# Kernel tuning notes

Hardware: AMD Instinct MI355X
Metric: run time of the kernel (lower is better)

The kernel has to match this reference:

```python
import jax, jax.numpy as jnp
import numpy as np

B, S = 1024, 512
V, E, H, T = 50000, 300, 800, 50


def setup_inputs() -> dict:
    key = jax.random.key(0)
    ks = jax.random.split(key, 8)
    ids = jax.random.randint(ks[0], (B, S), 0, V, dtype=jnp.int64 if jax.config.jax_enable_x64 else jnp.int32)
    return {
        "ids": ids,
        "rho": jax.random.normal(ks[1], (V, E), jnp.float32) * 0.02,
        "alpha": jax.random.normal(ks[2], (T, E), jnp.float32) * 0.02,
        "W1": jax.random.normal(ks[3], (E, H), jnp.float32) * 0.05,
        "b1": jnp.zeros((H,), jnp.float32),
        "Wmu": jax.random.normal(ks[4], (H, T), jnp.float32) * 0.05,
        "bmu": jnp.zeros((T,), jnp.float32),
        "Wlv": jax.random.normal(ks[5], (H, T), jnp.float32) * 0.05,
        "blv": jnp.zeros((T,), jnp.float32),
    }


def reference(ids, rho, alpha, W1, b1, Wmu, bmu, Wlv, blv):
    b, s = ids.shape
    v = rho.shape[0]
    # bag-of-words histogram: scatter-add instead of dense one_hot+reduce_sum
    bows = jnp.zeros((b, v), rho.dtype).at[jnp.arange(b)[:, None], ids].add(1.0)
    # zero out special tokens 1 and 2 (original: x * (1 - sum(one_hot([1,2]))))
    bows = bows.at[:, jnp.array([1, 2])].set(0.0)
    normal_bows = bows / jnp.sum(bows, axis=-1, keepdims=True)
    # encoder (eval mode: dropout is identity)
    x = jnp.einsum('bv,ve->be', normal_bows, rho)
    h = jax.nn.relu(x @ W1 + b1)
    mu_theta = h @ Wmu + bmu
    logsigma_theta = h @ Wlv + blv
    kl_theta = -0.5 * jnp.sum(1.0 + logsigma_theta - mu_theta**2 - jnp.exp(logsigma_theta), axis=-1)
    # reparameterize (eval/inference mode): z = mu
    theta = jax.nn.softmax(mu_theta, axis=-1)  # [B, T]
    beta = jax.nn.softmax(jnp.einsum('te,ve->tv', alpha, rho), axis=-1)  # [T, V]
    lookup = jnp.log(theta @ beta + 1e-5)  # [B, V]
    recon_loss = -jnp.sum(lookup * bows, axis=-1)
    loss = jnp.mean(recon_loss) + jnp.mean(kl_theta)
    return theta, loss
```

## Files before the change

kernel.cpp:

```cpp
#include <hip/hip_runtime.h>
#include <math.h>


#define Bn 1024
#define Sn 512
#define Vn 50000
#define En 300
#define Hn 800
#define Tn 50
#define KP 320
#define BSTR 64
#define W1FRAG_N (50 * 10 * 64 * 8)
#define WFRAG_N  (8 * 25 * 64 * 8)
#define NRANGE 8
#define K4B 3128

typedef __bf16 bf16x8 __attribute__((ext_vector_type(8)));
typedef float  f32x4  __attribute__((ext_vector_type(4)));
typedef float  f32x2  __attribute__((ext_vector_type(2)));

__device__ __forceinline__ float waveReduceSum(float v) {
    #pragma unroll
    for (int off = 32; off > 0; off >>= 1) v += __shfl_xor(v, off, 64);
    return v;
}
__device__ __forceinline__ float waveReduceMax(float v) {
    #pragma unroll
    for (int off = 32; off > 0; off >>= 1) v = fmaxf(v, __shfl_xor(v, off, 64));
    return v;
}
__device__ __forceinline__ unsigned short f2bf(float x) {
    unsigned u = __float_as_uint(x);
    return (unsigned short)((u + 0x7FFFu + ((u >> 16) & 1u)) >> 16);
}
__device__ __forceinline__ float bf_lo(unsigned u) { return __uint_as_float(u << 16); }
__device__ __forceinline__ float bf_hi(unsigned u) { return __uint_as_float(u & 0xFFFF0000u); }
__device__ __forceinline__ int lane_prefix(unsigned long long m) {
    return __builtin_amdgcn_mbcnt_hi((unsigned)(m >> 32),
           __builtin_amdgcn_mbcnt_lo((unsigned)m, 0));
}

#define PKACC(u) { \
    c0 += (f32x2){bf_lo((u).x), bf_hi((u).x)}; \
    c1 += (f32x2){bf_lo((u).y), bf_hi((u).y)}; \
    c2 += (f32x2){bf_lo((u).z), bf_hi((u).z)}; \
    c3 += (f32x2){bf_lo((u).w), bf_hi((u).w)}; }

__global__ __launch_bounds__(256) void ka2_init(
        const float* __restrict__ alpha, const float* __restrict__ W1,
        const float* __restrict__ Wmu, const float* __restrict__ Wlv,
        unsigned short* __restrict__ bfrag, unsigned short* __restrict__ w1frag,
        unsigned short* __restrict__ wfrag, float* __restrict__ topicsumR,
        float* __restrict__ loss) {
    const int gid = blockIdx.x * 256 + threadIdx.x;
    if (gid < 512) topicsumR[gid] = 0.f;
    if (gid == 520) *loss = 0.f;
    if (gid < 4 * 10 * 64 * 8) {
        int j = gid & 7;
        int lane = (gid >> 3) & 63;
        int rest = gid >> 9;
        int kt = rest % 10, w = rest / 10;
        int t = 16 * w + (lane & 15);
        int e = kt * 32 + (lane >> 4) * 8 + j;
        bfrag[gid] = (t < Tn && e < En) ? f2bf(alpha[t * En + e]) : (unsigned short)0;
    }
    if (gid < W1FRAG_N) {
        int j = gid & 7, lane = (gid >> 3) & 63, rest = gid >> 9;
        int kt = rest % 10, nt = rest / 10;
        int e = kt * 32 + (lane >> 4) * 8 + j;
        int hcol = nt * 16 + (lane & 15);
        w1frag[gid] = (e < En) ? f2bf(W1[e * Hn + hcol]) : (unsigned short)0;
    } else {
        int g2 = gid - W1FRAG_N;
        if (g2 < WFRAG_N) {
            int j = g2 & 7, lane = (g2 >> 3) & 63, rest = g2 >> 9;
            int kt = rest % 25, nt = rest / 25;
            int k = kt * 32 + (lane >> 4) * 8 + j;
            int t = (nt & 3) * 16 + (lane & 15);
            float val = 0.f;
            if (t < Tn) val = (nt < 4) ? Wmu[k * Tn + t] : Wlv[k * Tn + t];
            wfrag[g2] = f2bf(val);
        }
    }
}

__global__ __launch_bounds__(256) void kb4_beta(
        const float* __restrict__ rho, unsigned short* __restrict__ rhoh,
        const unsigned short* __restrict__ bfrag,
        unsigned int* __restrict__ betaU32, float* __restrict__ topicsumR) {
    __shared__ __align__(16) unsigned short xs[16 * 328];
    __shared__ unsigned short trans[16 * 66];
    const int x = blockIdx.x & 7;
    const int n = blockIdx.x >> 3;
    const int tile = ((x * 3125) >> 3) + n;
    if (tile >= (((x + 1) * 3125) >> 3)) return;
    const int tid = threadIdx.x;
    const int wave = tid >> 6, lane = tid & 63;
    const int quad = lane >> 4, l15 = lane & 15;
    const int v0 = tile * 16;
    for (int i = tid; i < 16 * 80; i += 256) {
        int row = i / 80, s4 = i - row * 80;
        ushort4 o = {0, 0, 0, 0};
        if (s4 < 75) {
            float4 r = *(const float4*)(rho + (size_t)(v0 + row) * En + s4 * 4);
            o.x = f2bf(r.x); o.y = f2bf(r.y); o.z = f2bf(r.z); o.w = f2bf(r.w);
        }
        *(ushort4*)&xs[row * 328 + s4 * 4] = o;
    }
    __syncthreads();
    for (int i = tid; i < 16 * 40; i += 256) {
        int row = i / 40, c8 = (i - row * 40) * 8;
        *(uint4*)(rhoh + (size_t)(v0 + row) * KP + c8) = *(const uint4*)&xs[row * 328 + c8];
    }
    const unsigned short* arow = xs + l15 * 328 + quad * 8;
    f32x4 acc = {0.f, 0.f, 0.f, 0.f};
    #pragma unroll
    for (int kt = 0; kt < 10; ++kt) {
        bf16x8 a = *(const bf16x8*)(arow + kt * 32);
        bf16x8 bv = *(const bf16x8*)(bfrag + ((wave * 10 + kt) * 64 + lane) * 8);
        acc = __builtin_amdgcn_mfma_f32_16x16x32_bf16(a, bv, acc, 0, 0, 0);
    }
    float ts = 0.f;
    #pragma unroll
    for (int r = 0; r < 4; ++r) {
        float ev = expf(acc[r]);
        ts += ev;
        trans[(quad * 4 + r) * 66 + 16 * wave + l15] = f2bf(ev);
    }
    ts += __shfl_xor(ts, 16, 64);
    ts += __shfl_xor(ts, 32, 64);
    const int t = 16 * wave + l15;
    if (lane < 16 && t < Tn)
        atomicAdd(&topicsumR[x * 64 + t], ts);
    __syncthreads();
    unsigned int* dst = betaU32 + (size_t)v0 * 32;
    const unsigned int* tr32 = (const unsigned int*)trans;
    for (int i = tid; i < 16 * 32; i += 256)
        dst[i] = tr32[(i >> 5) * 33 + (i & 31)];
}

__global__ __launch_bounds__(256) void kb1_gather(
        const unsigned short* __restrict__ rhoh, const int* __restrict__ ids,
        int* __restrict__ toks, int* __restrict__ cnt,
        float* __restrict__ xbarP) {
    __shared__ __align__(16) int sid[Sn];
    __shared__ int sfid[Sn];
    __shared__ __align__(16) float xred[4][320];
    __shared__ int scount, sfull;
    const int tid = threadIdx.x;
    const int wave = tid >> 6, lane = tid & 63;
    const int r = blockIdx.x & (NRANGE - 1), b = blockIdx.x >> 3;
    const int lo = ((r * 3125) >> 3) * 16;
    const int hi = (((r + 1) * 3125) >> 3) * 16;
    if (tid == 0) { scount = 0; sfull = 0; }
    __syncthreads();
    #pragma unroll
    for (int s0 = 0; s0 < Sn; s0 += 256) {
        int id = __builtin_nontemporal_load(&ids[b * Sn + s0 + tid]);
        bool val = (id != 1 && id != 2);
        bool inr = val && id >= lo && id < hi;
        unsigned long long mb = __ballot(inr);
        int pre = lane_prefix(mb);
        int wc = __popcll(mb);
        int base = 0;
        if (lane == 0 && wc) base = atomicAdd(&scount, wc);
        base = __shfl(base, 0, 64);
        if (inr) sid[base + pre] = id;
        if (r == 0) {
            unsigned long long fb = __ballot(val);
            int fpre = lane_prefix(fb);
            int fwc = __popcll(fb);
            int fbase = 0;
            if (lane == 0 && fwc) fbase = atomicAdd(&sfull, fwc);
            fbase = __shfl(fbase, 0, 64);
            if (val) sfid[fbase + fpre] = id;
        }
    }
    __syncthreads();
    if (r == 0) {
        const int nf = sfull;
        for (int i = tid; i < nf; i += 256) toks[b * Sn + i] = sfid[i];
        if (tid == 0) cnt[b] = nf;
    }
    const int m = scount;
    f32x2 c0 = {0.f, 0.f}, c1 = {0.f, 0.f}, c2 = {0.f, 0.f}, c3 = {0.f, 0.f};
    if (lane < 40) {
        const uint4* rb = (const uint4*)rhoh;
        int s = wave;
        for (; s + 12 < m; s += 16) {
            int i0 = sid[s], i1 = sid[s + 4], i2 = sid[s + 8], i3 = sid[s + 12];
            uint4 u0 = rb[(size_t)i0 * 40 + lane];
            uint4 u1 = rb[(size_t)i1 * 40 + lane];
            uint4 u2 = rb[(size_t)i2 * 40 + lane];
            uint4 u3 = rb[(size_t)i3 * 40 + lane];
            PKACC(u0); PKACC(u1); PKACC(u2); PKACC(u3);
        }
        for (; s < m; s += 4) {
            uint4 u = rb[(size_t)sid[s] * 40 + lane];
            PKACC(u);
        }
        float* xw = &xred[wave][lane * 8];
        *(float4*)(xw)     = (float4){c0[0], c0[1], c1[0], c1[1]};
        *(float4*)(xw + 4) = (float4){c2[0], c2[1], c3[0], c3[1]};
    }
    __syncthreads();
    float* xbp = xbarP + ((size_t)b * NRANGE + r) * KP;
    for (int c = tid; c < KP; c += 256)
        xbp[c] = xred[0][c] + xred[1][c] + xred[2][c] + xred[3][c];
}

__global__ __launch_bounds__(256) void ktail(
        const float* __restrict__ xbarP, const int* __restrict__ cnt,
        const unsigned short* __restrict__ w1frag, const float* __restrict__ b1,
        const unsigned short* __restrict__ wfrag,
        const float* __restrict__ bmu, const float* __restrict__ blv,
        float* __restrict__ theta, float* __restrict__ loss) {
    __shared__ unsigned short xs[16 * 328];
    __shared__ unsigned short hs[16 * 808];
    __shared__ float mlds[16 * 65];
    __shared__ float llds[16 * 65];
    __shared__ float invn[16];
    const int tid = threadIdx.x;
    const int wave = tid >> 6, lane = tid & 63;
    const int quad = lane >> 4, l15 = lane & 15;
    const int b0 = blockIdx.x * 16;
    if (tid < 16) invn[tid] = 1.0f / (float)cnt[b0 + tid];
    __syncthreads();
    for (int i = tid; i < 16 * (KP / 4); i += 256) {
        int row = i / (KP / 4), e4 = (i - row * (KP / 4)) * 4;
        const float* bp = xbarP + ((size_t)(b0 + row) * NRANGE) * KP + e4;
        float sx = 0.f, sy = 0.f, sz = 0.f, sw_ = 0.f;
        #pragma unroll
        for (int rr = 0; rr < NRANGE; ++rr) {
            float4 v = *(const float4*)(bp + rr * KP);
            sx += v.x; sy += v.y; sz += v.z; sw_ += v.w;
        }
        float in = invn[row];
        ushort4 o;
        o.x = f2bf(sx * in); o.y = f2bf(sy * in);
        o.z = f2bf(sz * in); o.w = f2bf(sw_ * in);
        *(ushort4*)&xs[row * 328 + e4] = o;
    }
    __syncthreads();
    {
        const unsigned short* arow = xs + l15 * 328 + quad * 8;
        for (int nt = wave; nt < 50; nt += 4) {
            f32x4 acc = {0.f, 0.f, 0.f, 0.f};
            #pragma unroll
            for (int kt = 0; kt < 10; ++kt) {
                bf16x8 a = *(const bf16x8*)(arow + kt * 32);
                bf16x8 bv = *(const bf16x8*)(w1frag + ((size_t)(nt * 10 + kt) * 64 + lane) * 8);
                acc = __builtin_amdgcn_mfma_f32_16x16x32_bf16(a, bv, acc, 0, 0, 0);
            }
            const int col = nt * 16 + l15;
            const float bias = b1[col];
            #pragma unroll
            for (int r = 0; r < 4; ++r)
                hs[(quad * 4 + r) * 808 + col] = f2bf(fmaxf(acc[r] + bias, 0.f));
        }
    }
    __syncthreads();
    {
        const unsigned short* arow = hs + l15 * 808 + quad * 8;
        f32x4 am = {0.f, 0.f, 0.f, 0.f}, al = {0.f, 0.f, 0.f, 0.f};
        #pragma unroll
        for (int kt = 0; kt < 25; ++kt) {
            bf16x8 a  = *(const bf16x8*)(arow + kt * 32);
            bf16x8 bm = *(const bf16x8*)(wfrag + ((size_t)(wave * 25 + kt) * 64 + lane) * 8);
            bf16x8 bl = *(const bf16x8*)(wfrag + ((size_t)((4 + wave) * 25 + kt) * 64 + lane) * 8);
            am = __builtin_amdgcn_mfma_f32_16x16x32_bf16(a, bm, am, 0, 0, 0);
            al = __builtin_amdgcn_mfma_f32_16x16x32_bf16(a, bl, al, 0, 0, 0);
        }
        const int t = wave * 16 + l15;
        const float bm_ = (t < Tn) ? bmu[t] : 0.f;
        const float bl_ = (t < Tn) ? blv[t] : 0.f;
        #pragma unroll
        for (int r = 0; r < 4; ++r) {
            int row = quad * 4 + r;
            mlds[row * 65 + t] = am[r] + bm_;
            llds[row * 65 + t] = al[r] + bl_;
        }
    }
    __syncthreads();
    const int tt = (lane < Tn) ? lane : (Tn - 1);
    const bool act = (lane < Tn);
    float klacc = 0.f;
    #pragma unroll
    for (int k = 0; k < 4; ++k) {
        int row = wave * 4 + k;
        float mu = mlds[row * 65 + tt];
        float lv = llds[row * 65 + tt];
        float m = waveReduceMax(act ? mu : -1e30f);
        float ex = act ? expf(mu - m) : 0.f;
        float ssum = waveReduceSum(ex);
        if (act) theta[(b0 + row) * Tn + lane] = ex / ssum;
        klacc += waveReduceSum(act ? (1.f + lv - mu * mu - expf(lv)) : 0.f);
    }
    if (lane == 0) atomicAdd(loss, -0.5f * klacc * (1.0f / (float)Bn));
}

__global__ __launch_bounds__(256) void k6_recon(
        const int* __restrict__ toks, const int* __restrict__ cnt,
        const float* __restrict__ theta, const float* __restrict__ topicsumR,
        const unsigned short* __restrict__ betaUh, float* __restrict__ loss) {
    __shared__ float sw[Tn];
    __shared__ float swred[4];
    const int b = blockIdx.x, tid = threadIdx.x;
    if (tid < Tn) {
        float z = 0.f;
        #pragma unroll
        for (int j = 0; j < 8; ++j) z += topicsumR[j * 64 + tid];
        sw[tid] = theta[b * Tn + tid] / z;
    }
    __syncthreads();
    float wr[Tn];
    #pragma unroll
    for (int t = 0; t < Tn; ++t) wr[t] = sw[t];
    float lsum = 0.f;
    const int n = cnt[b];
    for (int i = tid; i < n; i += 256) {
        int v = toks[b * Sn + i];
        const uint4* q = (const uint4*)(betaUh + (size_t)v * BSTR);
        float dot = 0.f;
        #pragma unroll
        for (int k = 0; k < 6; ++k) {
            uint4 u = q[k];
            int t = 8 * k;
            dot += wr[t]     * bf_lo(u.x) + wr[t + 1] * bf_hi(u.x);
            dot += wr[t + 2] * bf_lo(u.y) + wr[t + 3] * bf_hi(u.y);
            dot += wr[t + 4] * bf_lo(u.z) + wr[t + 5] * bf_hi(u.z);
            dot += wr[t + 6] * bf_lo(u.w) + wr[t + 7] * bf_hi(u.w);
        }
        unsigned d = ((const unsigned*)q)[24];
        dot += wr[48] * bf_lo(d) + wr[49] * bf_hi(d);
        lsum += logf(dot + 1e-5f);
    }
    float s = waveReduceSum(lsum);
    const int wave = tid >> 6, lane = tid & 63;
    if (lane == 0) swred[wave] = s;
    __syncthreads();
    if (tid == 0) {
        float tot = swred[0] + swred[1] + swred[2] + swred[3];
        atomicAdd(loss, -tot * (1.0f / (float)Bn));
    }
}

extern "C" void kernel_launch(void* const* d_in, const int* in_sizes, int n_in,
                              void* d_out, int out_size, void* d_ws, size_t ws_size,
                              hipStream_t stream) {
    const int*   ids   = (const int*)d_in[0];
    const float* rho   = (const float*)d_in[1];
    const float* alpha = (const float*)d_in[2];
    const float* W1    = (const float*)d_in[3];
    const float* b1    = (const float*)d_in[4];
    const float* Wmu   = (const float*)d_in[5];
    const float* bmu   = (const float*)d_in[6];
    const float* Wlv   = (const float*)d_in[7];
    const float* blv   = (const float*)d_in[8];

    float* theta = (float*)d_out;
    float* loss  = theta + Bn * Tn;

    char* w = (char*)d_ws;
    float* topicsumR = (float*)w;               w += 8 * 64 * 4;
    unsigned short* bfrag = (unsigned short*)w; w += 4 * 10 * 64 * 8 * 2;
    unsigned short* w1frag = (unsigned short*)w; w += (size_t)W1FRAG_N * 2;
    unsigned short* wfrag = (unsigned short*)w;  w += (size_t)WFRAG_N * 2;
    int*   cnt      = (int*)w;                  w += Bn * 4;
    int*   toks     = (int*)w;                  w += Bn * Sn * 4;
    float* xbarP    = (float*)w;                w += (size_t)Bn * NRANGE * KP * 4;
    unsigned short* rhoh = (unsigned short*)w;  w += (size_t)Vn * KP * 2;
    unsigned int* betaU32 = (unsigned int*)w;   w += (size_t)Vn * 128;

    const int k0grid = (W1FRAG_N + WFRAG_N + 255) / 256;
    ka2_init<<<k0grid, 256, 0, stream>>>(
        alpha, W1, Wmu, Wlv, bfrag, w1frag, wfrag, topicsumR, loss);
    kb4_beta<<<K4B, 256, 0, stream>>>(rho, rhoh, bfrag, betaU32, topicsumR);
    kb1_gather<<<Bn * NRANGE, 256, 0, stream>>>(rhoh, ids, toks, cnt, xbarP);
    ktail<<<64, 256, 0, stream>>>(xbarP, cnt, w1frag, b1, wfrag, bmu, blv,
                                  theta, loss);
    k6_recon<<<Bn, 256, 0, stream>>>(toks, cnt, theta, topicsumR,
                                     (const unsigned short*)betaU32, loss);
}
```

Baseline: 201.2 us.

## Fold init kernel into beta kernel and replace topic-sum atomics with per-tile partials

The separate init kernel goes away. The beta kernel now converts alpha to bf16 on the fly instead of reading precomputed fragments, and extra blocks appended to its grid build the W1 and Wmu/Wlv fragments. The per-range topic-sum atomics become plain per-tile writes, which a spare block in the tail kernel reduces. Loss zeroing moves into the gather kernel. This removes one launch and atomic contention, at the cost of redundant alpha conversion in every beta block and a serial 3125-tile reduction in one block.

Result: slower. 364.7 us (+81.3%).

```diff
diff --git a/kernel.cpp b/kernel.cpp
--- a/kernel.cpp
+++ b/kernel.cpp
@@ -14,6 +14,8 @@
 #define WFRAG_N  (8 * 25 * 64 * 8)
 #define NRANGE 8
 #define K4B 3128
+#define NTILE 3125
+#define FRAGB 1400
 
 typedef __bf16 bf16x8 __attribute__((ext_vector_type(8)));
 typedef float  f32x4  __attribute__((ext_vector_type(4)));
@@ -39,6 +41,12 @@
     return __builtin_amdgcn_mbcnt_hi((unsigned)(m >> 32),
            __builtin_amdgcn_mbcnt_lo((unsigned)m, 0));
 }
+__device__ __forceinline__ bf16x8 pack8(float4 a, float4 b) {
+    union { bf16x8 v; unsigned short s[8]; } u;
+    u.s[0] = f2bf(a.x); u.s[1] = f2bf(a.y); u.s[2] = f2bf(a.z); u.s[3] = f2bf(a.w);
+    u.s[4] = f2bf(b.x); u.s[5] = f2bf(b.y); u.s[6] = f2bf(b.z); u.s[7] = f2bf(b.w);
+    return u.v;
+}
 
 #define PKACC(u) { \
     c0 += (f32x2){bf_lo((u).x), bf_hi((u).x)}; \
@@ -46,55 +54,41 @@
     c2 += (f32x2){bf_lo((u).z), bf_hi((u).z)}; \
     c3 += (f32x2){bf_lo((u).w), bf_hi((u).w)}; }
 
-__global__ __launch_bounds__(256) void ka2_init(
-        const float* __restrict__ alpha, const float* __restrict__ W1,
-        const float* __restrict__ Wmu, const float* __restrict__ Wlv,
-        unsigned short* __restrict__ bfrag, unsigned short* __restrict__ w1frag,
-        unsigned short* __restrict__ wfrag, float* __restrict__ topicsumR,
-        float* __restrict__ loss) {
-    const int gid = blockIdx.x * 256 + threadIdx.x;
-    if (gid < 512) topicsumR[gid] = 0.f;
-    if (gid == 520) *loss = 0.f;
-    if (gid < 4 * 10 * 64 * 8) {
-        int j = gid & 7;
-        int lane = (gid >> 3) & 63;
-        int rest = gid >> 9;
-        int kt = rest % 10, w = rest / 10;
-        int t = 16 * w + (lane & 15);
-        int e = kt * 32 + (lane >> 4) * 8 + j;
-        bfrag[gid] = (t < Tn && e < En) ? f2bf(alpha[t * En + e]) : (unsigned short)0;
-    }
-    if (gid < W1FRAG_N) {
-        int j = gid & 7, lane = (gid >> 3) & 63, rest = gid >> 9;
-        int kt = rest % 10, nt = rest / 10;
-        int e = kt * 32 + (lane >> 4) * 8 + j;
-        int hcol = nt * 16 + (lane & 15);
-        w1frag[gid] = (e < En) ? f2bf(W1[e * Hn + hcol]) : (unsigned short)0;
-    } else {
-        int g2 = gid - W1FRAG_N;
-        if (g2 < WFRAG_N) {
-            int j = g2 & 7, lane = (g2 >> 3) & 63, rest = g2 >> 9;
-            int kt = rest % 25, nt = rest / 25;
-            int k = kt * 32 + (lane >> 4) * 8 + j;
-            int t = (nt & 3) * 16 + (lane & 15);
-            float val = 0.f;
-            if (t < Tn) val = (nt < 4) ? Wmu[k * Tn + t] : Wlv[k * Tn + t];
-            wfrag[g2] = f2bf(val);
-        }
-    }
-}
-
-__global__ __launch_bounds__(256) void kb4_beta(
-        const float* __restrict__ rho, unsigned short* __restrict__ rhoh,
-        const unsigned short* __restrict__ bfrag,
-        unsigned int* __restrict__ betaU32, float* __restrict__ topicsumR) {
+__global__ __launch_bounds__(256) void kbA_beta(
+        const float* __restrict__ rho, const float* __restrict__ alpha,
+        const float* __restrict__ W1, const float* __restrict__ Wmu,
+        const float* __restrict__ Wlv, unsigned short* __restrict__ rhoh,
+        unsigned int* __restrict__ betaU32, float* __restrict__ topicsumT,
+        unsigned short* __restrict__ w1frag, unsigned short* __restrict__ wfrag) {
     __shared__ __align__(16) unsigned short xs[16 * 328];
     __shared__ unsigned short trans[16 * 66];
+    const int tid = threadIdx.x;
+    if (blockIdx.x >= K4B) {
+        const int gid = (blockIdx.x - K4B) * 256 + tid;
+        if (gid < W1FRAG_N) {
+            int j = gid & 7, lane = (gid >> 3) & 63, rest = gid >> 9;
+            int kt = rest % 10, nt = rest / 10;
+            int e = kt * 32 + (lane >> 4) * 8 + j;
+            int hcol = nt * 16 + (lane & 15);
+            w1frag[gid] = (e < En) ? f2bf(W1[e * Hn + hcol]) : (unsigned short)0;
+        } else {
+            int g2 = gid - W1FRAG_N;
+            if (g2 < WFRAG_N) {
+                int j = g2 & 7, lane = (g2 >> 3) & 63, rest = g2 >> 9;
+                int kt = rest % 25, nt = rest / 25;
+                int k = kt * 32 + (lane >> 4) * 8 + j;
+                int t = (nt & 3) * 16 + (lane & 15);
+                float val = 0.f;
+                if (t < Tn) val = (nt < 4) ? Wmu[k * Tn + t] : Wlv[k * Tn + t];
+                wfrag[g2] = f2bf(val);
+            }
+        }
+        return;
+    }
     const int x = blockIdx.x & 7;
     const int n = blockIdx.x >> 3;
     const int tile = ((x * 3125) >> 3) + n;
     if (tile >= (((x + 1) * 3125) >> 3)) return;
-    const int tid = threadIdx.x;
     const int wave = tid >> 6, lane = tid & 63;
     const int quad = lane >> 4, l15 = lane & 15;
     const int v0 = tile * 16;
@@ -112,12 +106,27 @@
         int row = i / 40, c8 = (i - row * 40) * 8;
         *(uint4*)(rhoh + (size_t)(v0 + row) * KP + c8) = *(const uint4*)&xs[row * 328 + c8];
     }
+    const int tA = 16 * wave + l15;
+    const float* arowA = alpha + (size_t)tA * En;
     const unsigned short* arow = xs + l15 * 328 + quad * 8;
     f32x4 acc = {0.f, 0.f, 0.f, 0.f};
     #pragma unroll
     for (int kt = 0; kt < 10; ++kt) {
         bf16x8 a = *(const bf16x8*)(arow + kt * 32);
-        bf16x8 bv = *(const bf16x8*)(bfrag + ((wave * 10 + kt) * 64 + lane) * 8);
+        bf16x8 bv;
+        const int e0 = kt * 32 + quad * 8;
+        if (tA < Tn && e0 + 8 <= En) {
+            float4 f0 = *(const float4*)(arowA + e0);
+            float4 f1 = *(const float4*)(arowA + e0 + 4);
+            bv = pack8(f0, f1);
+        } else {
+            union { bf16x8 v; unsigned short s[8]; } u;
+            #pragma unroll
+            for (int j = 0; j < 8; ++j)
+                u.s[j] = (tA < Tn && e0 + j < En) ? f2bf(arowA[e0 + j])
+                                                  : (unsigned short)0;
+            bv = u.v;
+        }
         acc = __builtin_amdgcn_mfma_f32_16x16x32_bf16(a, bv, acc, 0, 0, 0);
     }
     float ts = 0.f;
@@ -130,8 +139,8 @@
     ts += __shfl_xor(ts, 16, 64);
     ts += __shfl_xor(ts, 32, 64);
     const int t = 16 * wave + l15;
-    if (lane < 16 && t < Tn)
-        atomicAdd(&topicsumR[x * 64 + t], ts);
+    if (lane < 16)
+        topicsumT[(size_t)tile * 64 + t] = ts;
     __syncthreads();
     unsigned int* dst = betaU32 + (size_t)v0 * 32;
     const unsigned int* tr32 = (const unsigned int*)trans;
@@ -142,7 +151,7 @@
 __global__ __launch_bounds__(256) void kb1_gather(
         const unsigned short* __restrict__ rhoh, const int* __restrict__ ids,
         int* __restrict__ toks, int* __restrict__ cnt,
-        float* __restrict__ xbarP) {
+        float* __restrict__ xbarP, float* __restrict__ loss) {
     __shared__ __align__(16) int sid[Sn];
     __shared__ int sfid[Sn];
     __shared__ __align__(16) float xred[4][320];
@@ -152,6 +161,7 @@
     const int r = blockIdx.x & (NRANGE - 1), b = blockIdx.x >> 3;
     const int lo = ((r * 3125) >> 3) * 16;
     const int hi = (((r + 1) * 3125) >> 3) * 16;
+    if (blockIdx.x == 0 && tid == 0) *loss = 0.f;
     if (tid == 0) { scount = 0; sfull = 0; }
     __syncthreads();
     #pragma unroll
@@ -214,6 +224,7 @@
         const unsigned short* __restrict__ w1frag, const float* __restrict__ b1,
         const unsigned short* __restrict__ wfrag,
         const float* __restrict__ bmu, const float* __restrict__ blv,
+        const float* __restrict__ topicsumT, float* __restrict__ topicsum,
         float* __restrict__ theta, float* __restrict__ loss) {
     __shared__ unsigned short xs[16 * 328];
     __shared__ unsigned short hs[16 * 808];
@@ -221,6 +232,18 @@
     __shared__ float llds[16 * 65];
     __shared__ float invn[16];
     const int tid = threadIdx.x;
+    if (blockIdx.x == 64) {
+        float* red = (float*)xs;
+        const int t = tid & 63, g = tid >> 6;
+        float s = 0.f;
+        for (int tile = g; tile < NTILE; tile += 4)
+            s += topicsumT[(size_t)tile * 64 + t];
+        red[g * 64 + t] = s;
+        __syncthreads();
+        if (tid < 64)
+            topicsum[tid] = red[tid] + red[64 + tid] + red[128 + tid] + red[192 + tid];
+        return;
+    }
     const int wave = tid >> 6, lane = tid & 63;
     const int quad = lane >> 4, l15 = lane & 15;
     const int b0 = blockIdx.x * 16;
@@ -301,17 +324,12 @@
 
 __global__ __launch_bounds__(256) void k6_recon(
         const int* __restrict__ toks, const int* __restrict__ cnt,
-        const float* __restrict__ theta, const float* __restrict__ topicsumR,
+        const float* __restrict__ theta, const float* __restrict__ topicsum,
         const unsigned short* __restrict__ betaUh, float* __restrict__ loss) {
     __shared__ float sw[Tn];
     __shared__ float swred[4];
     const int b = blockIdx.x, tid = threadIdx.x;
-    if (tid < Tn) {
-        float z = 0.f;
-        #pragma unroll
-        for (int j = 0; j < 8; ++j) z += topicsumR[j * 64 + tid];
-        sw[tid] = theta[b * Tn + tid] / z;
-    }
+    if (tid < Tn) sw[tid] = theta[b * Tn + tid] / topicsum[tid];
     __syncthreads();
     float wr[Tn];
     #pragma unroll
@@ -362,8 +380,8 @@
     float* loss  = theta + Bn * Tn;
 
     char* w = (char*)d_ws;
-    float* topicsumR = (float*)w;               w += 8 * 64 * 4;
-    unsigned short* bfrag = (unsigned short*)w; w += 4 * 10 * 64 * 8 * 2;
+    float* topicsumT = (float*)w;               w += (size_t)NTILE * 64 * 4;
+    float* topicsum  = (float*)w;               w += 64 * 4;
     unsigned short* w1frag = (unsigned short*)w; w += (size_t)W1FRAG_N * 2;
     unsigned short* wfrag = (unsigned short*)w;  w += (size_t)WFRAG_N * 2;
     int*   cnt      = (int*)w;                  w += Bn * 4;
@@ -372,13 +390,11 @@
     unsigned short* rhoh = (unsigned short*)w;  w += (size_t)Vn * KP * 2;
     unsigned int* betaU32 = (unsigned int*)w;   w += (size_t)Vn * 128;
 
-    const int k0grid = (W1FRAG_N + WFRAG_N + 255) / 256;
-    ka2_init<<<k0grid, 256, 0, stream>>>(
-        alpha, W1, Wmu, Wlv, bfrag, w1frag, wfrag, topicsumR, loss);
-    kb4_beta<<<K4B, 256, 0, stream>>>(rho, rhoh, bfrag, betaU32, topicsumR);
-    kb1_gather<<<Bn * NRANGE, 256, 0, stream>>>(rhoh, ids, toks, cnt, xbarP);
-    ktail<<<64, 256, 0, stream>>>(xbarP, cnt, w1frag, b1, wfrag, bmu, blv,
-                                  theta, loss);
-    k6_recon<<<Bn, 256, 0, stream>>>(toks, cnt, theta, topicsumR,
+    kbA_beta<<<K4B + FRAGB, 256, 0, stream>>>(
+        rho, alpha, W1, Wmu, Wlv, rhoh, betaU32, topicsumT, w1frag, wfrag);
+    kb1_gather<<<Bn * NRANGE, 256, 0, stream>>>(rhoh, ids, toks, cnt, xbarP, loss);
+    ktail<<<65, 256, 0, stream>>>(xbarP, cnt, w1frag, b1, wfrag, bmu, blv,
+                                  topicsumT, topicsum, theta, loss);
+    k6_recon<<<Bn, 256, 0, stream>>>(toks, cnt, theta, topicsum,
                                      (const unsigned short*)betaU32, loss);
 }
```
